# Performance work log

Measured on AMD Instinct MI355X. Metric: run time of the kernel, lower is better.

Reference implementation:

```python
import jax, jax.numpy as jnp
import numpy as np

B, N, INPUT_DIM, SELF_DIM = 8192, 96, 64, 16
HUMAN_DIM = INPUT_DIM - SELF_DIM  # 48


def setup_inputs() -> dict:
    key = jax.random.key(0)
    ks = jax.random.split(key, 8)
    inp = {
        "state": jax.random.normal(ks[0], (B, N, INPUT_DIM), dtype=jnp.float32),
        # t MLP: Linear(16,50) -> ReLU -> Linear(50,48)
        "t_w1": jax.random.normal(ks[1], (SELF_DIM, 50), dtype=jnp.float32) * 0.1,
        "t_b1": jnp.zeros((50,), dtype=jnp.float32),
        "t_w2": jax.random.normal(ks[2], (50, HUMAN_DIM), dtype=jnp.float32) * 0.1,
        "t_b2": jnp.zeros((HUMAN_DIM,), dtype=jnp.float32),
        # attention weight (scaled to keep softmax unsaturated)
        "w_a": jax.random.normal(ks[3], (HUMAN_DIM, HUMAN_DIM), dtype=jnp.float32) * 0.02,
        # graph-conv weights
        "w1": jax.random.normal(ks[4], (HUMAN_DIM, 64), dtype=jnp.float32) * 0.1,
        "w2": jax.random.normal(ks[5], (64, 64), dtype=jnp.float32) * 0.1,
        # value head: Linear(64,64) -> ReLU -> Linear(64,1)
        "v_w1": jax.random.normal(ks[6], (64, 64), dtype=jnp.float32) * 0.1,
        "v_b1": jnp.zeros((64,), dtype=jnp.float32),
        "v_w2": jax.random.normal(ks[7], (64, 1), dtype=jnp.float32) * 0.1,
        "v_b2": jnp.zeros((1,), dtype=jnp.float32),
    }
    return inp


def reference(state, t_w1, t_b1, t_w2, t_b2, w_a, w1, w2, v_w1, v_b1, v_w2, v_b2):
    # self-state MLP (t_mlp=True path), extra ReLU applied on MLP output
    self_state = state[:, 0, :SELF_DIM]                       # [B, S]
    human = state[:, :, SELF_DIM:]                            # [B, N, H]
    h = jax.nn.relu(self_state @ t_w1 + t_b1)                 # [B, 50]
    new_self = jax.nn.relu(h @ t_w2 + t_b2)[:, None, :]       # [B, 1, H]
    X = jnp.concatenate([new_self, human], axis=1)            # [B, N+1, H]
    # attention-weighted adjacency: softmax(X W_a X^T) over last dim
    scores = jnp.einsum('bnh,hk,bmk->bnm', X, w_a, X)         # [B, N+1, N+1]
    A = jax.nn.softmax(scores, axis=2)
    # two graph-conv layers (num_layer == 2, expand_x=False)
    h1 = jax.nn.relu(jnp.einsum('bnm,bmh,hk->bnk', A, X, w1))   # [B, N+1, 64]
    h2 = jax.nn.relu(jnp.einsum('bnm,bmh,hk->bnk', A, h1, w2))  # [B, N+1, 64]
    feat = h2[:, 0, :]                                        # [B, 64]
    # value head MLP (planning_mlp=True)
    value = jax.nn.relu(feat @ v_w1 + v_b1) @ v_w2 + v_b2     # [B, 1]
    return value
```

## Files before the change

### kernel.cpp

```cpp
#include <hip/hip_runtime.h>


#define XP (97 * 16)
#define ES 104
#define WS 56

typedef short bf16x8 __attribute__((ext_vector_type(8)));
typedef float f32x4 __attribute__((ext_vector_type(4)));

__device__ __forceinline__ unsigned rtne_hi(float f) {
    unsigned u = __float_as_uint(f);
    return (u + 0x7fffu + ((u >> 16) & 1u)) & 0xffff0000u;
}
__device__ __forceinline__ void split2(float f, unsigned short* h, unsigned short* l) {
    unsigned hb = rtne_hi(f);
    float r = f - __uint_as_float(hb);
    *h = (unsigned short)(hb >> 16);
    *l = (unsigned short)(__float_as_uint(r) >> 16);
}
__device__ __forceinline__ float bf2f(unsigned short u) {
    return __uint_as_float(((unsigned)u) << 16);
}
__device__ __forceinline__ bf16x8 ldf(const unsigned short* p) {
    return *(const bf16x8*)p;
}

__global__ void vnet_prep(const float* __restrict__ w_a, const float* __restrict__ w1,
                          unsigned short* __restrict__ ws) {
    unsigned short* waT_h = ws;
    unsigned short* waT_l = ws + 2304;
    unsigned short* w1T_h = ws + 4608;
    unsigned short* w1T_l = ws + 4608 + 3072;
    for (int i = threadIdx.x; i < 48 * 48; i += blockDim.x) {
        int c = i / 48, k = i % 48;
        unsigned short h, l; split2(w_a[k * 48 + c], &h, &l);
        waT_h[i] = h; waT_l[i] = l;
    }
    for (int i = threadIdx.x; i < 64 * 48; i += blockDim.x) {
        int lo = i / 48, j = i % 48;
        unsigned short h, l; split2(w1[j * 64 + lo], &h, &l);
        w1T_h[i] = h; w1T_l[i] = l;
    }
}

__global__ __launch_bounds__(256, 4)
void vnet_kernel(const float* __restrict__ state,
                 const float* __restrict__ t_w1, const float* __restrict__ t_b1,
                 const float* __restrict__ t_w2, const float* __restrict__ t_b2,
                 const float* __restrict__ w2,   const float* __restrict__ v_w1,
                 const float* __restrict__ v_b1, const float* __restrict__ v_w2,
                 const float* __restrict__ v_b2, const unsigned short* __restrict__ ws,
                 float* __restrict__ out)
{
    __shared__ __align__(16) unsigned short Xh[3 * XP], Xl[3 * XP];
    __shared__ __align__(16) unsigned short Eh[16 * ES], El[16 * ES];
    __shared__ __align__(16) unsigned short W0h[16 * WS], W0l[16 * WS];
    __shared__ __align__(16) unsigned short W1h[16 * WS], W1l[16 * WS];
    __shared__ float a0c[112];
    __shared__ float invb[16];
    __shared__ float e96[16];
    __shared__ float pacc[64];

    const unsigned short* waT_h = ws;
    const unsigned short* waT_l = ws + 2304;
    const unsigned short* w1T_h = ws + 4608;
    const unsigned short* w1T_l = ws + 4608 + 3072;

    const int tid  = threadIdx.x;
    const int w    = tid >> 6;
    const int lane = tid & 63;
    const int row  = lane & 15;
    const int quad = lane >> 4;
    const int b    = blockIdx.x;
    const float* sb = state + (size_t)b * (96 * 64);
    const bf16x8 ZF = {0, 0, 0, 0, 0, 0, 0, 0};

    if (tid < 16) pacc[tid] = sb[tid];
    for (int i = tid; i < 96 * 12; i += 256) {
        int r = i / 12, q = i % 12;
        float4 v = *(const float4*)(sb + r * 64 + 16 + 4 * q);
        unsigned short h0, l0, h1v, l1, h2, l2, h3, l3;
        split2(v.x, &h0, &l0); split2(v.y, &h1v, &l1);
        split2(v.z, &h2, &l2); split2(v.w, &h3, &l3);
        int m = 1 + r;
        int o = (q >> 2) * XP + m * 16 + (q & 3) * 4;
        *(uint2*)&Xh[o] = make_uint2((unsigned)h0 | ((unsigned)h1v << 16),
                                     (unsigned)h2 | ((unsigned)h3 << 16));
        *(uint2*)&Xl[o] = make_uint2((unsigned)l0 | ((unsigned)l1 << 16),
                                     (unsigned)l2 | ((unsigned)l3 << 16));
    }
    __syncthreads();

    if (tid < 50) {
        float a = t_b1[tid];
        #pragma unroll
        for (int i = 0; i < 16; ++i) a = fmaf(pacc[i], t_w1[i * 50 + tid], a);
        a0c[tid] = fmaxf(a, 0.f);
    }
    __syncthreads();
    if (tid < 48) {
        float a = t_b2[tid];
        for (int i = 0; i < 50; ++i) a = fmaf(a0c[i], t_w2[i * 48 + tid], a);
        unsigned short h, l; split2(fmaxf(a, 0.f), &h, &l);
        int o = (tid >> 4) * XP + (tid & 15);
        Xh[o] = h; Xl[o] = l;
    }
    if (tid >= 64 && tid < 128) pacc[tid - 64] = 0.f;
    if (tid >= 128 && tid < 143) a0c[tid - 31] = 0.f;
    __syncthreads();

    bf16x8 B4h[3], B4l[3];
    if (w < 3) {
        #pragma unroll
        for (int c3 = 0; c3 < 3; ++c3) {
            bf16x8 th, tl;
            #pragma unroll
            for (int j = 0; j < 8; ++j) {
                int e = w * XP + (32 * c3 + 8 * quad + j) * 16 + row;
                th[j] = (short)Xh[e];
                tl[j] = (short)Xl[e];
            }
            B4h[c3] = th;
            B4l[c3] = tl;
        }
    } else {
        #pragma unroll
        for (int c3 = 0; c3 < 3; ++c3) { B4h[c3] = ZF; B4l[c3] = ZF; }
    }

    {
        if (w < 3) {
            f32x4 acc = {0.f, 0.f, 0.f, 0.f};
            #pragma unroll
            for (int ch = 0; ch < 2; ++ch) {
                int kb = 16 * ch;
                int c = kb + quad * 8;
                int o = (c >> 4) * XP + row * 16 + (c & 15);
                bf16x8 ah = ldf(&Xh[o]);
                bf16x8 al = ldf(&Xl[o]);
                if (ch == 1 && quad < 2) { ah = ZF; al = ZF; }
                bf16x8 bh = ldf(waT_h + (16 * w + row) * 48 + kb + quad * 8);
                bf16x8 bl = ldf(waT_l + (16 * w + row) * 48 + kb + quad * 8);
                acc = __builtin_amdgcn_mfma_f32_16x16x32_bf16(ah, bh, acc, 0, 0, 0);
                acc = __builtin_amdgcn_mfma_f32_16x16x32_bf16(ah, bl, acc, 0, 0, 0);
                acc = __builtin_amdgcn_mfma_f32_16x16x32_bf16(al, bh, acc, 0, 0, 0);
            }
            #pragma unroll
            for (int r = 0; r < 4; ++r) {
                unsigned short h, l; split2(acc[r], &h, &l);
                W0h[(quad * 4 + r) * WS + 16 * w + row] = h;
                W0l[(quad * 4 + r) * WS + 16 * w + row] = l;
            }
        }
    }
    __syncthreads();
    {
        bf16x8 a0h = ldf(&W0h[row * WS + quad * 8]);
        bf16x8 a0l = ldf(&W0l[row * WS + quad * 8]);
        bf16x8 a1h = ldf(&W0h[row * WS + 16 + quad * 8]);
        bf16x8 a1l = ldf(&W0l[row * WS + 16 + quad * 8]);
        if (quad < 2) { a1h = ZF; a1l = ZF; }
        for (int t = w; t < 6; t += 4) {
            int m = 16 * t + row;
            f32x4 acc = {0.f, 0.f, 0.f, 0.f};
            int o0 = (quad >> 1) * XP + m * 16 + (quad & 1) * 8;
            bf16x8 bh = ldf(&Xh[o0]);
            bf16x8 bl = ldf(&Xl[o0]);
            acc = __builtin_amdgcn_mfma_f32_16x16x32_bf16(a0h, bh, acc, 0, 0, 0);
            acc = __builtin_amdgcn_mfma_f32_16x16x32_bf16(a0h, bl, acc, 0, 0, 0);
            acc = __builtin_amdgcn_mfma_f32_16x16x32_bf16(a0l, bh, acc, 0, 0, 0);
            bh = ldf(&Xh[o0 + XP]);
            bl = ldf(&Xl[o0 + XP]);
            acc = __builtin_amdgcn_mfma_f32_16x16x32_bf16(a1h, bh, acc, 0, 0, 0);
            acc = __builtin_amdgcn_mfma_f32_16x16x32_bf16(a1h, bl, acc, 0, 0, 0);
            acc = __builtin_amdgcn_mfma_f32_16x16x32_bf16(a1l, bh, acc, 0, 0, 0);
            #pragma unroll
            for (int r = 0; r < 4; ++r) {
                unsigned short h, l; split2(acc[r], &h, &l);
                Eh[(quad * 4 + r) * ES + m] = h;
                El[(quad * 4 + r) * ES + m] = l;
            }
        }
    }
    __syncthreads();

    for (int s = 0; s < 7; ++s) {
        unsigned short* Wsh = (s & 1) ? W1h : W0h;
        unsigned short* Wsl = (s & 1) ? W1l : W0l;
        unsigned short* Wnh = (s & 1) ? W0h : W1h;
        unsigned short* Wnl = (s & 1) ? W0l : W1l;

        if (s < 6 && w < 3) {
            f32x4 acc = {0.f, 0.f, 0.f, 0.f};
            int n = (s + 1) * 16 + row; int nc = n < 97 ? n : 96;
            #pragma unroll
            for (int ch = 0; ch < 2; ++ch) {
                int kb = 16 * ch;
                int c = kb + quad * 8;
                int o = (c >> 4) * XP + nc * 16 + (c & 15);
                bf16x8 ah = ldf(&Xh[o]);
                bf16x8 al = ldf(&Xl[o]);
                if (ch == 1 && quad < 2) { ah = ZF; al = ZF; }
                bf16x8 bh = ldf(waT_h + (16 * w + row) * 48 + kb + quad * 8);
                bf16x8 bl = ldf(waT_l + (16 * w + row) * 48 + kb + quad * 8);
                acc = __builtin_amdgcn_mfma_f32_16x16x32_bf16(ah, bh, acc, 0, 0, 0);
                acc = __builtin_amdgcn_mfma_f32_16x16x32_bf16(ah, bl, acc, 0, 0, 0);
                acc = __builtin_amdgcn_mfma_f32_16x16x32_bf16(al, bh, acc, 0, 0, 0);
            }
            #pragma unroll
            for (int r = 0; r < 4; ++r) {
                unsigned short h, l; split2(acc[r], &h, &l);
                Wnh[(quad * 4 + r) * WS + 16 * w + row] = h;
                Wnl[(quad * 4 + r) * WS + 16 * w + row] = l;
            }
        }
        {
            int rw = tid >> 4, mg = tid & 15;
            float s96 = 0.f;
            #pragma unroll
            for (int kk = 0; kk < 3; ++kk) {
                int c = mg + 16 * kk;
                float xw = bf2f(Wsh[rw * WS + c]) + bf2f(Wsl[rw * WS + c]);
                float xv = bf2f(Xh[kk * XP + 1536 + mg]) + bf2f(Xl[kk * XP + 1536 + mg]);
                s96 = fmaf(xw, xv, s96);
            }
            s96 += __shfl_xor(s96, 1); s96 += __shfl_xor(s96, 2);
            s96 += __shfl_xor(s96, 4); s96 += __shfl_xor(s96, 8);
            float e0 = __expf(s96);
            float sum = (mg == 0) ? e0 : 0.f;
            if (mg == 0) {
                e96[rw] = e0;
                if (s == 0 && rw == 0) a0c[96] = e0;
            }
            for (int m = mg; m < 96; m += 16) {
                int o = rw * ES + m;
                float f = bf2f(Eh[o]) + bf2f(El[o]);
                float e = __expf(f);
                sum += e;
                unsigned short h, l; split2(e, &h, &l);
                Eh[o] = h; El[o] = l;
                if (s == 0 && rw == 0) a0c[m] = e;
            }
            sum += __shfl_xor(sum, 1); sum += __shfl_xor(sum, 2);
            sum += __shfl_xor(sum, 4); sum += __shfl_xor(sum, 8);
            if (mg == 0) invb[rw] = 1.f / sum;
        }
        __syncthreads();

        if (w < 3) {
            f32x4 acc = {0.f, 0.f, 0.f, 0.f};
            #pragma unroll
            for (int c3 = 0; c3 < 3; ++c3) {
                int mb = 32 * c3;
                bf16x8 ah = ldf(&Eh[row * ES + mb + quad * 8]);
                bf16x8 al = ldf(&El[row * ES + mb + quad * 8]);
                acc = __builtin_amdgcn_mfma_f32_16x16x32_bf16(ah, B4h[c3], acc, 0, 0, 0);
                acc = __builtin_amdgcn_mfma_f32_16x16x32_bf16(ah, B4l[c3], acc, 0, 0, 0);
                acc = __builtin_amdgcn_mfma_f32_16x16x32_bf16(al, B4h[c3], acc, 0, 0, 0);
            }
            int j = 16 * w + row;
            float xv = bf2f(Xh[w * XP + 1536 + row]) + bf2f(Xl[w * XP + 1536 + row]);
            #pragma unroll
            for (int r = 0; r < 4; ++r) {
                float v = fmaf(e96[quad * 4 + r], xv, acc[r]) * invb[quad * 4 + r];
                unsigned short h, l; split2(v, &h, &l);
                Wsh[(quad * 4 + r) * WS + j] = h;
                Wsl[(quad * 4 + r) * WS + j] = l;
            }
        } else if (s == 0) {
            float iv0 = invb[0];
            for (int m = lane; m < 97; m += 64) a0c[m] *= iv0;
        }
        __syncthreads();

        {
            f32x4 acc = {0.f, 0.f, 0.f, 0.f};
            #pragma unroll
            for (int ch = 0; ch < 2; ++ch) {
                int kb = 16 * ch;
                bf16x8 ah = ldf(&Wsh[row * WS + kb + quad * 8]);
                bf16x8 al = ldf(&Wsl[row * WS + kb + quad * 8]);
                if (ch == 1 && quad < 2) { ah = ZF; al = ZF; }
                bf16x8 bh = ldf(w1T_h + (16 * w + row) * 48 + kb + quad * 8);
                bf16x8 bl = ldf(w1T_l + (16 * w + row) * 48 + kb + quad * 8);
                acc = __builtin_amdgcn_mfma_f32_16x16x32_bf16(ah, bh, acc, 0, 0, 0);
                acc = __builtin_amdgcn_mfma_f32_16x16x32_bf16(ah, bl, acc, 0, 0, 0);
                acc = __builtin_amdgcn_mfma_f32_16x16x32_bf16(al, bh, acc, 0, 0, 0);
            }
            float part = 0.f;
            #pragma unroll
            for (int r = 0; r < 4; ++r)
                part += fmaxf(acc[r], 0.f) * a0c[s * 16 + quad * 4 + r];
            part += __shfl_xor(part, 16);
            part += __shfl_xor(part, 32);
            if (quad == 0) pacc[16 * w + row] += part;
        }
        if (s < 6) {
            bf16x8 a0h = ldf(&Wnh[row * WS + quad * 8]);
            bf16x8 a0l = ldf(&Wnl[row * WS + quad * 8]);
            bf16x8 a1h = ldf(&Wnh[row * WS + 16 + quad * 8]);
            bf16x8 a1l = ldf(&Wnl[row * WS + 16 + quad * 8]);
            if (quad < 2) { a1h = ZF; a1l = ZF; }
            for (int t = w; t < 6; t += 4) {
                int m = 16 * t + row;
                f32x4 acc = {0.f, 0.f, 0.f, 0.f};
                int o0 = (quad >> 1) * XP + m * 16 + (quad & 1) * 8;
                bf16x8 bh = ldf(&Xh[o0]);
                bf16x8 bl = ldf(&Xl[o0]);
                acc = __builtin_amdgcn_mfma_f32_16x16x32_bf16(a0h, bh, acc, 0, 0, 0);
                acc = __builtin_amdgcn_mfma_f32_16x16x32_bf16(a0h, bl, acc, 0, 0, 0);
                acc = __builtin_amdgcn_mfma_f32_16x16x32_bf16(a0l, bh, acc, 0, 0, 0);
                bh = ldf(&Xh[o0 + XP]);
                bl = ldf(&Xl[o0 + XP]);
                acc = __builtin_amdgcn_mfma_f32_16x16x32_bf16(a1h, bh, acc, 0, 0, 0);
                acc = __builtin_amdgcn_mfma_f32_16x16x32_bf16(a1h, bl, acc, 0, 0, 0);
                acc = __builtin_amdgcn_mfma_f32_16x16x32_bf16(a1l, bh, acc, 0, 0, 0);
                #pragma unroll
                for (int r = 0; r < 4; ++r) {
                    unsigned short h, l; split2(acc[r], &h, &l);
                    Eh[(quad * 4 + r) * ES + m] = h;
                    El[(quad * 4 + r) * ES + m] = l;
                }
            }
        }
        __syncthreads();
    }

    float* featb = a0c;
    if (tid < 64) {
        float a = 0.f;
        #pragma unroll 8
        for (int l = 0; l < 64; ++l) a = fmaf(pacc[l], w2[l * 64 + tid], a);
        featb[tid] = fmaxf(a, 0.f);
    }
    __syncthreads();
    if (tid < 64) {
        float a = v_b1[tid];
        #pragma unroll 8
        for (int c = 0; c < 64; ++c) a = fmaf(featb[c], v_w1[c * 64 + tid], a);
        float qd = fmaxf(a, 0.f) * v_w2[tid];
        #pragma unroll
        for (int d = 32; d >= 1; d >>= 1) qd += __shfl_xor(qd, d);
        if (tid == 0) out[b] = qd + v_b2[0];
    }
}

extern "C" void kernel_launch(void* const* d_in, const int* in_sizes, int n_in,
                              void* d_out, int out_size, void* d_ws, size_t ws_size,
                              hipStream_t stream) {
    (void)n_in; (void)ws_size; (void)out_size;
    const float* state = (const float*)d_in[0];
    const float* t_w1  = (const float*)d_in[1];
    const float* t_b1  = (const float*)d_in[2];
    const float* t_w2  = (const float*)d_in[3];
    const float* t_b2  = (const float*)d_in[4];
    const float* w_a   = (const float*)d_in[5];
    const float* w1    = (const float*)d_in[6];
    const float* w2    = (const float*)d_in[7];
    const float* v_w1  = (const float*)d_in[8];
    const float* v_b1  = (const float*)d_in[9];
    const float* v_w2  = (const float*)d_in[10];
    const float* v_b2  = (const float*)d_in[11];
    unsigned short* ws = (unsigned short*)d_ws;
    const int nb = in_sizes[0] / (96 * 64);

    vnet_prep<<<1, 256, 0, stream>>>(w_a, w1, ws);
    vnet_kernel<<<nb, 256, 0, stream>>>(state, t_w1, t_b1, t_w2, t_b2, w2,
                                        v_w1, v_b1, v_w2, v_b2, ws, (float*)d_out);
}
```

Baseline: 485.7 us.

## Fuse softmax exp and row sums into score MFMA epilogue, drop E low part

Moves the exponential and the per-row partial sums of the attention softmax into the epilogue of the score MFMA, so the separate pass that reread, exponentiated and rewrote the score tile in shared memory goes away. The exponentials are now stored only as a single rounded bf16 instead of a hi/lo pair, which removes one shared array and one of the three MFMAs per chunk in the A·X product. The occupancy hint is raised from 4 to 5 blocks per CU, which the smaller LDS footprint may allow. The cost is lower precision on the softmax weights (bf16 only) and some extra shuffle reductions per tile.

After: 519.4 us. 6.9% more time.

```diff
diff --git a/kernel.cpp b/kernel.cpp
--- a/kernel.cpp
+++ b/kernel.cpp
@@ -17,6 +17,9 @@
     float r = f - __uint_as_float(hb);
     *h = (unsigned short)(hb >> 16);
     *l = (unsigned short)(__float_as_uint(r) >> 16);
+}
+__device__ __forceinline__ unsigned short rtne16(float f) {
+    return (unsigned short)(rtne_hi(f) >> 16);
 }
 __device__ __forceinline__ float bf2f(unsigned short u) {
     return __uint_as_float(((unsigned)u) << 16);
@@ -43,7 +46,7 @@
     }
 }
 
-__global__ __launch_bounds__(256, 4)
+__global__ __launch_bounds__(256, 5)
 void vnet_kernel(const float* __restrict__ state,
                  const float* __restrict__ t_w1, const float* __restrict__ t_b1,
                  const float* __restrict__ t_w2, const float* __restrict__ t_b2,
@@ -53,13 +56,14 @@
                  float* __restrict__ out)
 {
     __shared__ __align__(16) unsigned short Xh[3 * XP], Xl[3 * XP];
-    __shared__ __align__(16) unsigned short Eh[16 * ES], El[16 * ES];
+    __shared__ __align__(16) unsigned short Eh[16 * ES];
     __shared__ __align__(16) unsigned short W0h[16 * WS], W0l[16 * WS];
     __shared__ __align__(16) unsigned short W1h[16 * WS], W1l[16 * WS];
     __shared__ float a0c[112];
     __shared__ float invb[16];
     __shared__ float e96[16];
     __shared__ float pacc[64];
+    __shared__ float psum[64];
 
     const unsigned short* waT_h = ws;
     const unsigned short* waT_l = ws + 2304;
@@ -160,6 +164,7 @@
         bf16x8 a1h = ldf(&W0h[row * WS + 16 + quad * 8]);
         bf16x8 a1l = ldf(&W0l[row * WS + 16 + quad * 8]);
         if (quad < 2) { a1h = ZF; a1l = ZF; }
+        float ps0 = 0.f, ps1 = 0.f, ps2 = 0.f, ps3 = 0.f;
         for (int t = w; t < 6; t += 4) {
             int m = 16 * t + row;
             f32x4 acc = {0.f, 0.f, 0.f, 0.f};
@@ -174,12 +179,25 @@
             acc = __builtin_amdgcn_mfma_f32_16x16x32_bf16(a1h, bh, acc, 0, 0, 0);
             acc = __builtin_amdgcn_mfma_f32_16x16x32_bf16(a1h, bl, acc, 0, 0, 0);
             acc = __builtin_amdgcn_mfma_f32_16x16x32_bf16(a1l, bh, acc, 0, 0, 0);
-            #pragma unroll
-            for (int r = 0; r < 4; ++r) {
-                unsigned short h, l; split2(acc[r], &h, &l);
-                Eh[(quad * 4 + r) * ES + m] = h;
-                El[(quad * 4 + r) * ES + m] = l;
-            }
+            float e0v = __expf(acc[0]), e1v = __expf(acc[1]);
+            float e2v = __expf(acc[2]), e3v = __expf(acc[3]);
+            Eh[(quad * 4 + 0) * ES + m] = rtne16(e0v);
+            Eh[(quad * 4 + 1) * ES + m] = rtne16(e1v);
+            Eh[(quad * 4 + 2) * ES + m] = rtne16(e2v);
+            Eh[(quad * 4 + 3) * ES + m] = rtne16(e3v);
+            if (quad == 0) a0c[m] = e0v;
+            ps0 += e0v; ps1 += e1v; ps2 += e2v; ps3 += e3v;
+        }
+        #pragma unroll
+        for (int d = 1; d < 16; d <<= 1) {
+            ps0 += __shfl_xor(ps0, d); ps1 += __shfl_xor(ps1, d);
+            ps2 += __shfl_xor(ps2, d); ps3 += __shfl_xor(ps3, d);
+        }
+        if (row == 0) {
+            psum[w * 16 + quad * 4 + 0] = ps0;
+            psum[w * 16 + quad * 4 + 1] = ps1;
+            psum[w * 16 + quad * 4 + 2] = ps2;
+            psum[w * 16 + quad * 4 + 3] = ps3;
         }
     }
     __syncthreads();
@@ -227,23 +245,15 @@
             s96 += __shfl_xor(s96, 1); s96 += __shfl_xor(s96, 2);
             s96 += __shfl_xor(s96, 4); s96 += __shfl_xor(s96, 8);
             float e0 = __expf(s96);
-            float sum = (mg == 0) ? e0 : 0.f;
+            float sum = (mg < 4) ? psum[mg * 16 + rw] : 0.f;
+            if (mg == 0) sum += e0;
+            sum += __shfl_xor(sum, 1); sum += __shfl_xor(sum, 2);
+            sum += __shfl_xor(sum, 4); sum += __shfl_xor(sum, 8);
             if (mg == 0) {
                 e96[rw] = e0;
+                invb[rw] = 1.f / sum;
                 if (s == 0 && rw == 0) a0c[96] = e0;
             }
-            for (int m = mg; m < 96; m += 16) {
-                int o = rw * ES + m;
-                float f = bf2f(Eh[o]) + bf2f(El[o]);
-                float e = __expf(f);
-                sum += e;
-                unsigned short h, l; split2(e, &h, &l);
-                Eh[o] = h; El[o] = l;
-                if (s == 0 && rw == 0) a0c[m] = e;
-            }
-            sum += __shfl_xor(sum, 1); sum += __shfl_xor(sum, 2);
-            sum += __shfl_xor(sum, 4); sum += __shfl_xor(sum, 8);
-            if (mg == 0) invb[rw] = 1.f / sum;
         }
         __syncthreads();
 
@@ -253,10 +263,8 @@
             for (int c3 = 0; c3 < 3; ++c3) {
                 int mb = 32 * c3;
                 bf16x8 ah = ldf(&Eh[row * ES + mb + quad * 8]);
-                bf16x8 al = ldf(&El[row * ES + mb + quad * 8]);
                 acc = __builtin_amdgcn_mfma_f32_16x16x32_bf16(ah, B4h[c3], acc, 0, 0, 0);
                 acc = __builtin_amdgcn_mfma_f32_16x16x32_bf16(ah, B4l[c3], acc, 0, 0, 0);
-                acc = __builtin_amdgcn_mfma_f32_16x16x32_bf16(al, B4h[c3], acc, 0, 0, 0);
             }
             int j = 16 * w + row;
             float xv = bf2f(Xh[w * XP + 1536 + row]) + bf2f(Xl[w * XP + 1536 + row]);
@@ -301,6 +309,7 @@
             bf16x8 a1h = ldf(&Wnh[row * WS + 16 + quad * 8]);
             bf16x8 a1l = ldf(&Wnl[row * WS + 16 + quad * 8]);
             if (quad < 2) { a1h = ZF; a1l = ZF; }
+            float ps0 = 0.f, ps1 = 0.f, ps2 = 0.f, ps3 = 0.f;
             for (int t = w; t < 6; t += 4) {
                 int m = 16 * t + row;
                 f32x4 acc = {0.f, 0.f, 0.f, 0.f};
@@ -315,12 +324,24 @@
                 acc = __builtin_amdgcn_mfma_f32_16x16x32_bf16(a1h, bh, acc, 0, 0, 0);
                 acc = __builtin_amdgcn_mfma_f32_16x16x32_bf16(a1h, bl, acc, 0, 0, 0);
                 acc = __builtin_amdgcn_mfma_f32_16x16x32_bf16(a1l, bh, acc, 0, 0, 0);
-                #pragma unroll
-                for (int r = 0; r < 4; ++r) {
-                    unsigned short h, l; split2(acc[r], &h, &l);
-                    Eh[(quad * 4 + r) * ES + m] = h;
-                    El[(quad * 4 + r) * ES + m] = l;
-                }
+                float e0v = __expf(acc[0]), e1v = __expf(acc[1]);
+                float e2v = __expf(acc[2]), e3v = __expf(acc[3]);
+                Eh[(quad * 4 + 0) * ES + m] = rtne16(e0v);
+                Eh[(quad * 4 + 1) * ES + m] = rtne16(e1v);
+                Eh[(quad * 4 + 2) * ES + m] = rtne16(e2v);
+                Eh[(quad * 4 + 3) * ES + m] = rtne16(e3v);
+                ps0 += e0v; ps1 += e1v; ps2 += e2v; ps3 += e3v;
+            }
+            #pragma unroll
+            for (int d = 1; d < 16; d <<= 1) {
+                ps0 += __shfl_xor(ps0, d); ps1 += __shfl_xor(ps1, d);
+                ps2 += __shfl_xor(ps2, d); ps3 += __shfl_xor(ps3, d);
+            }
+            if (row == 0) {
+                psum[w * 16 + quad * 4 + 0] = ps0;
+                psum[w * 16 + quad * 4 + 1] = ps1;
+                psum[w * 16 + quad * 4 + 2] = ps2;
+                psum[w * 16 + quad * 4 + 3] = ps3;
             }
         }
         __syncthreads();
```
